# Optimization experiments

Measured on AMD Instinct MI355X. Metric: run time of the kernel, lower is better.

## Reference

```python
import jax, jax.numpy as jnp
import numpy as np

SCALE = 100.0
ALPHA_MEM = 0.9
ALPHA_MEM_OUT = 0.9
ALPHA_R = 0.85
ALPHA_X = 0.95
ALPHA_P = 0.95
ALPHA_D = 0.95
WMIN = 0.0
WMAX = 2.0


@jax.custom_vjp
def spike_fn(x):
    # SurrGradSpike.forward: heaviside(x)
    return (x > 0).astype(x.dtype)

def _spike_fwd(x):
    return spike_fn(x), x

def _spike_bwd(x, g):
    # SurrGradSpike.backward: g / (scale*|x| + 1)^2
    return (g / (SCALE * jnp.abs(x) + 1.0) ** 2,)

spike_fn.defvjp(_spike_fwd, _spike_bwd)


def setup_inputs() -> dict:
    key = jax.random.key(0)
    ks = jax.random.split(key, 8)
    B, T, NI, N, NO, D = 8, 64, 256, 512, 32, 4
    inputs = jax.random.normal(ks[0], (B, T, NI), jnp.float32)
    w = jax.random.normal(ks[1], (N, N), jnp.float32) * (0.1 / np.sqrt(N))
    w_in = jax.random.normal(ks[2], (NI, N), jnp.float32) * (1.0 / np.sqrt(NI))
    w_out = jax.random.normal(ks[3], (N, NO), jnp.float32) * (1.0 / np.sqrt(N))
    # each synapse (e,o) assigned exactly one delay bin -> one-hot delay map (D,N,N)
    delay_idx = jax.random.randint(ks[4], (N, N), 0, D)
    dmap = jax.nn.one_hot(delay_idx, D, axis=0, dtype=jnp.float32)
    delays = jnp.array([1, 2, 3, 5], jnp.int32)
    w_signs = jnp.where(jnp.arange(N) < (4 * N) // 5, 1.0, -1.0).astype(jnp.float32)
    p = jax.random.uniform(ks[5], (N,), jnp.float32, minval=-0.5, maxval=0.5)
    A_p = jax.random.uniform(ks[6], (N, N), jnp.float32, minval=0.0, maxval=1e-3)
    A_d = jax.random.uniform(ks[7], (N, N), jnp.float32, minval=0.0, maxval=1e-3)
    return dict(inputs=inputs, w=w, w_in=w_in, w_out=w_out, dmap=dmap,
                delays=delays, w_signs=w_signs, p=p, A_p=A_p, A_d=A_d)


def _snn_forward(inputs, w, w_in, w_out, dmap, delays, w_signs, p, A_p, A_d):
    B, T, _ = inputs.shape
    N = w.shape[0]
    dt = inputs.dtype
    # epoch state
    inp = jnp.einsum('btc,cn->btn', inputs, w_in)          # (B,T,N)
    W = dmap * (w_signs[:, None] * jnp.abs(w))             # (D,N,N)
    p_depr = (p < 0).astype(dt)

    mem = jnp.zeros((B, N), dt)
    w_p = jnp.zeros((B, N), dt)
    x_bar = jnp.zeros((B, N), dt)
    u_pot = jnp.zeros((B, N), dt)
    u_dep = jnp.zeros((B, N), dt)
    w_stdp = jnp.ones((B, N, N), dt)
    rec_out = jnp.zeros((T, B, N), dt)
    rec_wp = jnp.zeros((T, B, N), dt)
    rec_xb = jnp.zeros((T, B, N), dt)

    def step(carry, xt):
        mem, w_p, x_bar, u_pot, u_dep, w_stdp, rec_out, rec_wp, rec_xb = carry
        t, inp_t = xt
        # mark_spikes + record_state (records pre-update values)
        spike = spike_fn(mem - 1.0)
        rec_out = rec_out.at[t].set(spike)
        rec_wp = rec_wp.at[t].set(w_p)
        rec_xb = rec_xb.at[t].set(x_bar)
        # delayed gathers; negative torch indices hit zero-initialized tail -> %T
        idx = (t - delays) % T
        out_del = jnp.take(rec_out, idx, axis=0)           # (D,B,N)
        wp_del = jnp.take(rec_wp, idx, axis=0)
        xb_del = jnp.take(rec_xb, idx, axis=0)
        # synaptic input
        syn_p = out_del * (1.0 + wp_del)
        syn = jnp.einsum('dbe,deo,beo->bo', syn_p, W, w_stdp)
        # STP
        dw_p = spike * p * (1.0 + p_depr * w_p)
        w_p = w_p * ALPHA_R + dw_p
        # STDP (uses pre-update u_dep/u_pot/mem)
        X = jnp.einsum('dbe,deo->beo', out_del, dmap)
        dW_dep = X * A_d[None] * jax.nn.relu(u_dep)[:, None, :]
        xbar_d = jnp.einsum('dbe,deo->beo', xb_del, dmap)
        dW_pot = xbar_d * A_p[None] * (jax.lax.stop_gradient(spike) * jax.nn.relu(u_pot))[:, None, :]
        x_bar = ALPHA_X * x_bar + (1.0 - ALPHA_X) * jax.lax.stop_gradient(spike)
        u_pot = ALPHA_P * u_pot + (1.0 - ALPHA_P) * mem
        u_dep = ALPHA_D * u_dep + (1.0 - ALPHA_D) * mem
        w_stdp = jnp.clip(w_stdp + dW_pot - dW_dep, WMIN, WMAX)
        # membrane integration with spike reset (detached)
        mem = ALPHA_MEM * mem + inp_t + syn - jax.lax.stop_gradient(spike)
        return (mem, w_p, x_bar, u_pot, u_dep, w_stdp, rec_out, rec_wp, rec_xb), None

    carry = (mem, w_p, x_bar, u_pot, u_dep, w_stdp, rec_out, rec_wp, rec_xb)
    xs = (jnp.arange(T), jnp.swapaxes(inp, 0, 1))
    carry, _ = jax.lax.scan(jax.checkpoint(step), carry, xs)
    rec_out = carry[6]                                     # (T,B,N)
    # readout: leaky integrator over projected spikes
    h2 = jnp.einsum('btn,no->bto', jnp.swapaxes(rec_out, 0, 1), w_out)

    def ro_step(o, h):
        o = ALPHA_MEM_OUT * o + h
        return o, o

    _, readout = jax.lax.scan(ro_step, jnp.zeros((B, h2.shape[-1]), dt),
                              jnp.swapaxes(h2, 0, 1))
    return jnp.swapaxes(readout, 0, 1)                     # (B,T,n_outputs)


def reference(inputs, w, w_in, w_out, dmap, delays, w_signs, p, A_p, A_d):
    return _snn_forward(inputs, w, w_in, w_out, dmap, delays, w_signs, p, A_p, A_d)
```

## Files before the change

### kernel.cpp

```cpp
#include <hip/hip_runtime.h>
#include <stdint.h>


#define B  8
#define T  64
#define NI 256
#define NN 512
#define NO 32
#define DD 4

#define NBLK 256
#define TPB  256
#define OPB  16
#define SPL  32
#define EPAD 516

#define REC_ELEMS (T*B*NN)

__device__ __forceinline__ unsigned long long rec_load(const unsigned long long* p) {
    return __hip_atomic_load(p, __ATOMIC_RELAXED, __HIP_MEMORY_SCOPE_AGENT);
}
__device__ __forceinline__ void rec_store(unsigned long long* p, unsigned long long v) {
    __hip_atomic_store(p, v, __ATOMIC_RELAXED, __HIP_MEMORY_SCOPE_AGENT);
}
__device__ __forceinline__ bool is_sentinel(unsigned long long v) {
    return (unsigned int)(v >> 32) == 0xFFFFFFFFu;
}

__global__ __launch_bounds__(TPB, 1)
void snn_main(const float* __restrict__ inputs,
              const float* __restrict__ w,
              const float* __restrict__ w_in,
              const float* __restrict__ dmap,
              const int*   __restrict__ delays,
              const float* __restrict__ w_signs,
              const float* __restrict__ p,
              const float* __restrict__ A_p,
              const float* __restrict__ A_d,
              unsigned long long* __restrict__ rec)
{
    __shared__ float2 sxq[DD*EPAD];
    __shared__ float  inp_s[T*OPB];
    __shared__ float  red[64];

    const int tid     = threadIdx.x;
    const int bid     = blockIdx.x;
    const int b       = bid & 7;
    const int chunk   = bid >> 3;
    const int o_base  = chunk * OPB;
    const int o_local = tid & 15;
    const int e_grp   = tid >> 4;
    const int o       = o_base + o_local;

    if (tid < OPB) {
        rec_store(rec + (size_t)(0*B + b)*NN + o_base + tid, 0ull);
    }

    float wv[SPL], ap[SPL], ad[SPL], ws[SPL];
    int   laddr[SPL];
    #pragma unroll
    for (int i = 0; i < SPL; ++i) {
        const int e = e_grp + 16*i;
        wv[i] = w_signs[e] * fabsf(w[e*NN + o]);
        ap[i] = A_p[e*NN + o];
        ad[i] = A_d[e*NN + o];
        int d = 0;
        if (dmap[1*NN*NN + e*NN + o] != 0.0f) d = 1;
        if (dmap[2*NN*NN + e*NN + o] != 0.0f) d = 2;
        if (dmap[3*NN*NN + e*NN + o] != 0.0f) d = 3;
        ws[i]    = 1.0f;
        laddr[i] = (d*EPAD + e) * 8;
    }
    int del[DD];
    #pragma unroll
    for (int d = 0; d < DD; ++d) del[d] = delays[d];

    {
        float* win = (float*)sxq;
        for (int k = tid; k < NI*OPB; k += TPB) {
            const int c = k >> 4, oo = k & 15;
            win[c*OPB + oo] = w_in[c*NN + o_base + oo];
        }
        __syncthreads();
        #pragma unroll
        for (int j = 0; j < 4; ++j) {
            const int tj = e_grp*4 + j;
            const float* inrow = inputs + (size_t)(b*T + tj)*NI;
            float a = 0.f;
            for (int c = 0; c < NI; ++c) a += inrow[c] * win[c*OPB + o_local];
            inp_s[tj*OPB + o_local] = a;
        }
        __syncthreads();
    }

    #pragma unroll
    for (int d = 0; d < DD; ++d) {
        sxq[d*EPAD + tid]       = make_float2(0.f, 0.f);
        sxq[d*EPAD + 256 + tid] = make_float2(0.f, 0.f);
    }
    __syncthreads();

    float mem = 0.f, w_p = 0.f, x_bar = 0.f, u_pot = 0.f, u_dep = 0.f;
    const float p_o  = p[o];
    const float pd_o = (p_o < 0.f) ? 1.f : 0.f;

    unsigned long long pf[DD][2];

    for (int t = 0; t < T; ++t) {
        if (t + 1 < T) {
            #pragma unroll
            for (int d = 0; d < DD; ++d) {
                if (del[d] > 1 && t + 1 >= del[d]) {
                    const int s = (t + 1 - del[d]) & 63;
                    const unsigned long long* src = rec + (size_t)(s*B + b)*NN + tid;
                    pf[d][0] = rec_load(src);
                    pf[d][1] = rec_load(src + 256);
                }
            }
        }

        const float spike = (mem > 1.0f) ? 1.0f : 0.0f;
        const float pg  = spike * fmaxf(u_pot, 0.f);
        const float udr = fmaxf(u_dep, 0.f);
        float acc = 0.f;
        #pragma unroll
        for (int i = 0; i < SPL; ++i) {
            const float2 v = *(const float2*)((const char*)sxq + laddr[i]);
            acc = fmaf(v.x, wv[i]*ws[i], acc);
            const unsigned int xu = __float_as_uint(v.y);
            const float dep = ((int)xu < 0) ? ad[i]*udr : 0.f;
            const float pot = (ap[i]*pg) * fabsf(v.y);
            ws[i] = fminf(fmaxf(ws[i] + pot - dep, 0.f), 2.f);
        }
        float a2 = acc + __shfl_xor(acc, 16);
        a2 += __shfl_xor(a2, 32);
        if ((tid & 63) < 16) red[(tid >> 6)*16 + o_local] = a2;
        __syncthreads();
        const float syn = red[o_local] + red[16 + o_local] + red[32 + o_local] + red[48 + o_local];

        const float wp_new = 0.85f*w_p + spike * p_o * (1.f + pd_o*w_p);
        const float xb_new = 0.95f*x_bar + 0.05f*spike;
        u_pot = 0.95f*u_pot + 0.05f*mem;
        u_dep = 0.95f*u_dep + 0.05f*mem;
        mem   = 0.9f*mem + inp_s[t*OPB + o_local] + syn - spike;
        w_p   = wp_new;
        x_bar = xb_new;

        if (t + 1 < T && tid < OPB) {
            const float spike1 = (mem > 1.0f) ? 1.0f : 0.0f;
            const float sp = spike1 * (1.f + w_p);
            const unsigned int xu = __float_as_uint(x_bar) | (spike1 != 0.f ? 0x80000000u : 0u);
            const unsigned long long pk =
                ((unsigned long long)xu << 32) | (unsigned int)__float_as_uint(sp);
            rec_store(rec + (size_t)((t+1)*B + b)*NN + o_base + tid, pk);
        }

        if (t + 1 < T) {
            #pragma unroll
            for (int d = 0; d < DD; ++d) {
                unsigned long long v0 = 0ull, v1 = 0ull;
                if (t + 1 >= del[d]) {
                    const int s = (t + 1 - del[d]) & 63;
                    const unsigned long long* src = rec + (size_t)(s*B + b)*NN + tid;
                    if (del[d] > 1) { v0 = pf[d][0]; v1 = pf[d][1]; }
                    else            { v0 = rec_load(src); v1 = rec_load(src + 256); }
                    int guard = 0;
                    while (is_sentinel(v0)) {
                        __builtin_amdgcn_s_sleep(1);
                        v0 = rec_load(src);
                        if (++guard > (1 << 24)) break;
                    }
                    guard = 0;
                    while (is_sentinel(v1)) {
                        __builtin_amdgcn_s_sleep(1);
                        v1 = rec_load(src + 256);
                        if (++guard > (1 << 24)) break;
                    }
                }
                sxq[d*EPAD + tid] =
                    make_float2(__uint_as_float((unsigned int)v0),
                                __uint_as_float((unsigned int)(v0 >> 32)));
                sxq[d*EPAD + 256 + tid] =
                    make_float2(__uint_as_float((unsigned int)v1),
                                make_float2(0.f,0.f).x + __uint_as_float((unsigned int)(v1 >> 32)));
            }
        }
        __syncthreads();
    }
}

__global__ __launch_bounds__(256)
void snn_h2(const unsigned long long* __restrict__ rec,
            const float* __restrict__ w_out,
            float* __restrict__ h2)
{
    const int bt = blockIdx.x;
    const int b = bt >> 6, t = bt & 63;
    const int tid = threadIdx.x;
    const int o = tid & 31, g = tid >> 5;
    const unsigned long long* ro = rec + (size_t)(t*B + b)*NN + g*64;
    float a = 0.f;
    #pragma unroll 8
    for (int j = 0; j < 64; ++j)
        if ((long long)ro[j] < 0) a += w_out[(g*64 + j)*NO + o];
    __shared__ float r2[8][NO];
    r2[g][o] = a;
    __syncthreads();
    if (tid < NO) {
        float s = 0.f;
        #pragma unroll
        for (int gg = 0; gg < 8; ++gg) s += r2[gg][tid];
        h2[bt*NO + tid] = s;
    }
}

__global__ void snn_scan(const float* __restrict__ h2, float* __restrict__ out)
{
    const int tid = threadIdx.x;
    const int b = tid >> 5, o = tid & 31;
    float st = 0.f;
    for (int t = 0; t < T; ++t) {
        st = 0.9f*st + h2[(b*T + t)*NO + o];
        out[(b*T + t)*NO + o] = st;
    }
}

extern "C" void kernel_launch(void* const* d_in, const int* in_sizes, int n_in,
                              void* d_out, int out_size, void* d_ws, size_t ws_size,
                              hipStream_t stream)
{
    const float* inputs  = (const float*)d_in[0];
    const float* w       = (const float*)d_in[1];
    const float* w_in    = (const float*)d_in[2];
    const float* w_out   = (const float*)d_in[3];
    const float* dmap    = (const float*)d_in[4];
    const int*   delays  = (const int*)  d_in[5];
    const float* w_signs = (const float*)d_in[6];
    const float* p       = (const float*)d_in[7];
    const float* A_p     = (const float*)d_in[8];
    const float* A_d     = (const float*)d_in[9];

    char* wsb = (char*)d_ws;
    unsigned long long* rec = (unsigned long long*)wsb;
    float* h2 = (float*)(wsb + (size_t)REC_ELEMS*8);

    hipMemsetAsync(rec, 0xFF, (size_t)REC_ELEMS*8, stream);

    hipLaunchKernelGGL(snn_main, dim3(NBLK), dim3(TPB), 0, stream,
                       inputs, w, w_in, dmap, delays, w_signs, p, A_p, A_d, rec);
    hipLaunchKernelGGL(snn_h2, dim3(B*T), dim3(256), 0, stream,
                       rec, w_out, h2);
    hipLaunchKernelGGL(snn_scan, dim3(1), dim3(256), 0, stream,
                       h2, (float*)d_out);
}
```

Measured before the change: 275.8 us.

## Fuse readout projection and leaky scan into main kernel; use volatile loads for polling

Each block records its 16 neurons' spike bits per timestep in shared memory, then projects them through its slice of w_out and atomically accumulates into h2. The last block for each batch, found with an atomic counter, runs the leaky readout scan. This removes two extra kernel launches and the re-read of the record buffer. Polling loads switch to plain volatile loads and fall back to agent-scope atomics only after retries, and stores are written twice. Cross-block visibility under the volatile path is less certain, and float atomic accumulation order is nondeterministic.

```diff
diff --git a/kernel.cpp b/kernel.cpp
--- a/kernel.cpp
+++ b/kernel.cpp
@@ -17,10 +17,14 @@
 
 #define REC_ELEMS (T*B*NN)
 
-__device__ __forceinline__ unsigned long long rec_load(const unsigned long long* p) {
+__device__ __forceinline__ unsigned long long rec_load_agent(const unsigned long long* p) {
     return __hip_atomic_load(p, __ATOMIC_RELAXED, __HIP_MEMORY_SCOPE_AGENT);
 }
-__device__ __forceinline__ void rec_store(unsigned long long* p, unsigned long long v) {
+__device__ __forceinline__ unsigned long long rec_load_fast(const unsigned long long* p) {
+    return *(const volatile unsigned long long*)p;
+}
+__device__ __forceinline__ void rec_store_pub(unsigned long long* p, unsigned long long v) {
+    *(volatile unsigned long long*)p = v;
     __hip_atomic_store(p, v, __ATOMIC_RELAXED, __HIP_MEMORY_SCOPE_AGENT);
 }
 __device__ __forceinline__ bool is_sentinel(unsigned long long v) {
@@ -31,17 +35,25 @@
 void snn_main(const float* __restrict__ inputs,
               const float* __restrict__ w,
               const float* __restrict__ w_in,
+              const float* __restrict__ w_out,
               const float* __restrict__ dmap,
               const int*   __restrict__ delays,
               const float* __restrict__ w_signs,
               const float* __restrict__ p,
               const float* __restrict__ A_p,
               const float* __restrict__ A_d,
-              unsigned long long* __restrict__ rec)
+              unsigned long long* __restrict__ rec,
+              float* __restrict__ h2buf,
+              unsigned int* __restrict__ cnt,
+              float* __restrict__ out)
 {
     __shared__ float2 sxq[DD*EPAD];
     __shared__ float  inp_s[T*OPB];
     __shared__ float  red[64];
+    __shared__ unsigned int spikebits_s[T];
+    __shared__ float  wout16_s[OPB*NO];
+    __shared__ float  h2_s[T*NO];
+    __shared__ int    last_s;
 
     const int tid     = threadIdx.x;
     const int bid     = blockIdx.x;
@@ -53,8 +65,9 @@
     const int o       = o_base + o_local;
 
     if (tid < OPB) {
-        rec_store(rec + (size_t)(0*B + b)*NN + o_base + tid, 0ull);
-    }
+        rec_store_pub(rec + (size_t)(0*B + b)*NN + o_base + tid, 0ull);
+    }
+    if (tid == 0) spikebits_s[0] = 0u;
 
     float wv[SPL], ap[SPL], ad[SPL], ws[SPL];
     int   laddr[SPL];
@@ -113,8 +126,8 @@
                 if (del[d] > 1 && t + 1 >= del[d]) {
                     const int s = (t + 1 - del[d]) & 63;
                     const unsigned long long* src = rec + (size_t)(s*B + b)*NN + tid;
-                    pf[d][0] = rec_load(src);
-                    pf[d][1] = rec_load(src + 256);
+                    pf[d][0] = rec_load_fast(src);
+                    pf[d][1] = rec_load_fast(src + 256);
                 }
             }
         }
@@ -152,7 +165,9 @@
             const unsigned int xu = __float_as_uint(x_bar) | (spike1 != 0.f ? 0x80000000u : 0u);
             const unsigned long long pk =
                 ((unsigned long long)xu << 32) | (unsigned int)__float_as_uint(sp);
-            rec_store(rec + (size_t)((t+1)*B + b)*NN + o_base + tid, pk);
+            rec_store_pub(rec + (size_t)((t+1)*B + b)*NN + o_base + tid, pk);
+            const unsigned long long bal = __ballot(spike1 != 0.0f);
+            if (tid == 0) spikebits_s[t+1] = (unsigned int)bal;
         }
 
         if (t + 1 < T) {
@@ -163,17 +178,17 @@
                     const int s = (t + 1 - del[d]) & 63;
                     const unsigned long long* src = rec + (size_t)(s*B + b)*NN + tid;
                     if (del[d] > 1) { v0 = pf[d][0]; v1 = pf[d][1]; }
-                    else            { v0 = rec_load(src); v1 = rec_load(src + 256); }
+                    else            { v0 = rec_load_fast(src); v1 = rec_load_fast(src + 256); }
                     int guard = 0;
                     while (is_sentinel(v0)) {
                         __builtin_amdgcn_s_sleep(1);
-                        v0 = rec_load(src);
+                        v0 = (guard < 2) ? rec_load_fast(src) : rec_load_agent(src);
                         if (++guard > (1 << 24)) break;
                     }
                     guard = 0;
                     while (is_sentinel(v1)) {
                         __builtin_amdgcn_s_sleep(1);
-                        v1 = rec_load(src + 256);
+                        v1 = (guard < 2) ? rec_load_fast(src + 256) : rec_load_agent(src + 256);
                         if (++guard > (1 << 24)) break;
                     }
                 }
@@ -182,46 +197,48 @@
                                 __uint_as_float((unsigned int)(v0 >> 32)));
                 sxq[d*EPAD + 256 + tid] =
                     make_float2(__uint_as_float((unsigned int)v1),
-                                make_float2(0.f,0.f).x + __uint_as_float((unsigned int)(v1 >> 32)));
+                                __uint_as_float((unsigned int)(v1 >> 32)));
             }
         }
         __syncthreads();
     }
-}
-
-__global__ __launch_bounds__(256)
-void snn_h2(const unsigned long long* __restrict__ rec,
-            const float* __restrict__ w_out,
-            float* __restrict__ h2)
-{
-    const int bt = blockIdx.x;
-    const int b = bt >> 6, t = bt & 63;
-    const int tid = threadIdx.x;
-    const int o = tid & 31, g = tid >> 5;
-    const unsigned long long* ro = rec + (size_t)(t*B + b)*NN + g*64;
-    float a = 0.f;
-    #pragma unroll 8
-    for (int j = 0; j < 64; ++j)
-        if ((long long)ro[j] < 0) a += w_out[(g*64 + j)*NO + o];
-    __shared__ float r2[8][NO];
-    r2[g][o] = a;
+
+    for (int k = tid; k < OPB*NO; k += TPB)
+        wout16_s[k] = w_out[(o_base + (k >> 5))*NO + (k & 31)];
+    __syncthreads();
+
+    const int g  = tid >> 5;
+    const int oo = tid & 31;
+    #pragma unroll
+    for (int j = 0; j < 8; ++j) {
+        const int t = g*8 + j;
+        const unsigned int bits = spikebits_s[t];
+        float a = 0.f;
+        #pragma unroll
+        for (int i = 0; i < OPB; ++i)
+            if (bits & (1u << i)) a += wout16_s[i*NO + oo];
+        if (a != 0.f) atomicAdd(h2buf + ((size_t)b*T + t)*NO + oo, a);
+    }
+    __threadfence();
+    __syncthreads();
+    if (tid == 0) last_s = (atomicAdd(cnt + b, 1u) == 31u) ? 1 : 0;
+    __syncthreads();
+    if (!last_s) return;
+
+    __threadfence();
+    #pragma unroll
+    for (int j = 0; j < 8; ++j) {
+        const int t = g*8 + j;
+        h2_s[t*NO + oo] = __hip_atomic_load(h2buf + ((size_t)b*T + t)*NO + oo,
+                                            __ATOMIC_RELAXED, __HIP_MEMORY_SCOPE_AGENT);
+    }
     __syncthreads();
     if (tid < NO) {
-        float s = 0.f;
-        #pragma unroll
-        for (int gg = 0; gg < 8; ++gg) s += r2[gg][tid];
-        h2[bt*NO + tid] = s;
-    }
-}
-
-__global__ void snn_scan(const float* __restrict__ h2, float* __restrict__ out)
-{
-    const int tid = threadIdx.x;
-    const int b = tid >> 5, o = tid & 31;
-    float st = 0.f;
-    for (int t = 0; t < T; ++t) {
-        st = 0.9f*st + h2[(b*T + t)*NO + o];
-        out[(b*T + t)*NO + o] = st;
+        float st = 0.f;
+        for (int t = 0; t < T; ++t) {
+            st = 0.9f*st + h2_s[t*NO + tid];
+            out[((size_t)b*T + t)*NO + tid] = st;
+        }
     }
 }
 
@@ -242,14 +259,13 @@
 
     char* wsb = (char*)d_ws;
     unsigned long long* rec = (unsigned long long*)wsb;
-    float* h2 = (float*)(wsb + (size_t)REC_ELEMS*8);
+    float* h2buf = (float*)(wsb + (size_t)REC_ELEMS*8);
+    unsigned int* cnt = (unsigned int*)(wsb + (size_t)REC_ELEMS*8 + (size_t)B*T*NO*4);
 
     hipMemsetAsync(rec, 0xFF, (size_t)REC_ELEMS*8, stream);
+    hipMemsetAsync(h2buf, 0, (size_t)B*T*NO*4 + (size_t)B*4, stream);
 
     hipLaunchKernelGGL(snn_main, dim3(NBLK), dim3(TPB), 0, stream,
-                       inputs, w, w_in, dmap, delays, w_signs, p, A_p, A_d, rec);
-    hipLaunchKernelGGL(snn_h2, dim3(B*T), dim3(256), 0, stream,
-                       rec, w_out, h2);
-    hipLaunchKernelGGL(snn_scan, dim3(1), dim3(256), 0, stream,
-                       h2, (float*)d_out);
-}
+                       inputs, w, w_in, w_out, dmap, delays, w_signs, p, A_p, A_d,
+                       rec, h2buf, cnt, (float*)d_out);
+}
```

Measured after the change: 323.4 us. 17.3% more time.
